# Kernel optimization log

Measured on AMD Instinct MI355X. Metric: run time of the kernel, lower is better.

The kernel has to match this reference:

```python
import jax, jax.numpy as jnp
from jax import lax
import numpy as np

# Hyperparameters (module defaults)
MIP_K = 31
P_LO, P_HI = 0.01, 0.99
ALPHA = 0.15
MU = 10.0
PD_ITERS = 30
TAU = 0.125
SIG_PD = 0.125
THETA = 1.0
EPS = 1e-6


def _forward_grad(u):
    # forward differences, zero-padded on the far edge -> same shape as u
    dx = jnp.pad(u[..., :, 1:] - u[..., :, :-1], ((0, 0), (0, 0), (0, 0), (0, 1)))
    dy = jnp.pad(u[..., 1:, :] - u[..., :-1, :], ((0, 0), (0, 0), (0, 1), (0, 0)))
    return dx, dy


def _divergence(px, py):
    # backward-difference divergence (adjoint of forward grad)
    div_x = px - jnp.pad(px[..., :, :-1], ((0, 0), (0, 0), (0, 0), (1, 0)))
    div_y = py - jnp.pad(py[..., :-1, :], ((0, 0), (0, 0), (1, 0), (0, 0)))
    return div_x + div_y


def _max_pool(x, k):
    # stride-1 max pool with -inf padding (matches torch F.max_pool2d semantics)
    pad = k // 2
    return lax.reduce_window(
        x, -jnp.inf, lax.max,
        window_dimensions=(1, 1, k, k),
        window_strides=(1, 1, 1, 1),
        padding=((0, 0), (0, 0), (pad, pad), (pad, pad)))


def setup_inputs() -> dict:
    key = jax.random.key(0)
    Iy = jax.random.uniform(key, (16, 3, 512, 512), dtype=jnp.float32)
    return {"Iy": Iy}


def reference(Iy):
    R, G, Bc = Iy[:, 0:1], Iy[:, 1:2], Iy[:, 2:3]

    # MIP coarse depth
    Rmax = _max_pool(R, MIP_K)
    GBmax = jnp.maximum(_max_pool(G, MIP_K), _max_pool(Bc, MIP_K))
    x = jnp.abs(Rmax - GBmax) + R

    # robust per-image percentile normalization to [0,1]
    B = x.shape[0]
    flat = x.reshape(B, -1)
    lo = jnp.quantile(flat, P_LO, axis=1)[:, None, None, None]
    hi = jnp.quantile(flat, P_HI, axis=1)[:, None, None, None]
    N_hat = jnp.clip((x - lo) / (hi - lo + EPS), 0.0, 1.0)

    # fixed edge weights from grad(N_hat), sigma = per-image median grad magnitude
    dxh, dyh = _forward_grad(N_hat)
    grad_mag = jnp.sqrt(dxh * dxh + dyh * dyh + EPS)
    sigma = jnp.maximum(
        jnp.quantile(grad_mag.reshape(B, -1), 0.5, axis=1), EPS)[:, None, None, None]
    Wx = 1.0 + MU * jnp.exp(-jnp.abs(dxh) / sigma)
    Wy = 1.0 + MU * jnp.exp(-jnp.abs(dyh) / sigma)

    # Chambolle-Pock primal-dual iterations for weighted TV-L2
    def step(carry, _):
        u, u_bar, px, py = carry
        dx, dy = _forward_grad(u_bar)
        px = jnp.clip(px + SIG_PD * dx, -ALPHA * Wx, ALPHA * Wx)
        py = jnp.clip(py + SIG_PD * dy, -ALPHA * Wy, ALPHA * Wy)
        v = u + TAU * _divergence(px, py)
        u_new = (v + TAU * N_hat) / (1.0 + TAU)
        u_bar = u_new + THETA * (u_new - u)
        return (u_new, u_bar, px, py), None

    z = jnp.zeros_like(N_hat)
    (u, _, _, _), _ = lax.scan(step, (N_hat, N_hat, z, z), None, length=PD_ITERS)
    return jnp.clip(u, 0.0, 1.0)
```

## Files before the change

### kernel.cpp

```cpp
#include <hip/hip_runtime.h>
#include <math.h>

#define B_ 16
#define W_ 512
#define H_ 512
#define S_ (W_*H_)
#define ALPHA_ 0.15f
#define MU_ 10.0f
#define TAU_ 0.125f
#define SIG_ 0.125f
#define EPS_ 1e-6f
#define INV1PT_ (1.0f/(1.0f+TAU_))
#define NBINS 4096
#define BINSCALE 2048.0f
#define BINW (1.0f/2048.0f)

__global__ __launch_bounds__(256) void hmax_kernel(const float* __restrict__ Iy,
                                                   float* __restrict__ Rh,
                                                   float* __restrict__ GBh){
  __shared__ float bufA[2][544], bufB[2][544];
  int t = threadIdx.x;
  int b = blockIdx.x >> 9;
  int i = blockIdx.x & 511;
  const float* row = Iy + (size_t)b*3*S_ + (size_t)i*W_;
  for (int p = t; p < 544; p += 256){
    int idx = p - 16;
    bool v = (idx >= 0) && (idx < 512);
    bufA[0][p] = v ? row[idx] : -1e30f;
    bufA[1][p] = v ? fmaxf(row[S_+idx], row[2*S_+idx]) : -1e30f;
  }
  __syncthreads();
  float (*src)[544] = bufA; float (*dst)[544] = bufB;
  const int ds[5] = {1, 2, 4, 8, 15};
  #pragma unroll
  for (int sstep = 0; sstep < 5; ++sstep){
    int d = ds[sstep];
    for (int p = t; p < 544; p += 256){
      int q = min(p + d, 543);
      dst[0][p] = fmaxf(src[0][p], src[0][q]);
      dst[1][p] = fmaxf(src[1][p], src[1][q]);
    }
    __syncthreads();
    float (*tmp)[544] = src; src = dst; dst = tmp;
  }
  size_t o = (size_t)b*S_ + (size_t)i*W_;
  for (int p = t; p < 512; p += 256){
    Rh[o+p]  = src[0][p+1];
    GBh[o+p] = src[1][p+1];
  }
}

__global__ __launch_bounds__(256) void vscan_fwd_kernel(const float* __restrict__ Rh,
                                                        const float* __restrict__ GBh,
                                                        float* __restrict__ Rf,
                                                        float* __restrict__ Gf){
  int gid = blockIdx.x*256 + threadIdx.x;
  int col = gid & 8191;
  int c   = gid >> 13;
  int b = col >> 9, j = col & 511;
  int i0 = c*31, i1 = min(i0+31, H_);
  size_t base = (size_t)b*S_ + j;
  float rR = -1e30f, rG = -1e30f;
  for (int i = i0; i < i1; ++i){
    size_t o = base + (size_t)i*W_;
    rR = fmaxf(rR, Rh[o]); rG = fmaxf(rG, GBh[o]);
    Rf[o] = rR; Gf[o] = rG;
  }
}

__global__ __launch_bounds__(256) void vscan_bwd_kernel(const float* __restrict__ Rh,
                                                        const float* __restrict__ GBh,
                                                        const float* __restrict__ Rf,
                                                        const float* __restrict__ Gf,
                                                        const float* __restrict__ Iy,
                                                        float* __restrict__ xo,
                                                        unsigned int* __restrict__ hist){
  __shared__ unsigned int h[NBINS];
  int t = threadIdx.x;
  for (int p = t; p < NBINS; p += 256) h[p] = 0u;
  __syncthreads();
  int gid = blockIdx.x*256 + t;
  int col = gid & 8191;
  int c   = gid >> 13;
  int b = col >> 9, j = col & 511;
  int half = j >> 8;
  int i0 = c*31, i1 = min(i0+31, H_);
  size_t base = (size_t)b*S_ + j;
  const float* IyR = Iy + (size_t)b*3*S_ + j;
  float lR = -1e30f, lG = -1e30f;
  for (int i = i1-1; i >= i0; --i){
    size_t o64 = base + (size_t)i*W_;
    lR = fmaxf(lR, Rh[o64]); lG = fmaxf(lG, GBh[o64]);
    int o = i + 15;
    if (o < H_){
      int bi = min(i + 30, H_-1);
      size_t ob = base + (size_t)bi*W_;
      float mR = fmaxf(lR, Rf[ob]);
      float mG = fmaxf(lG, Gf[ob]);
      float xv = fabsf(mR - mG) + IyR[(size_t)o*W_];
      xo[base + (size_t)o*W_] = xv;
      int bin = (int)(xv*BINSCALE);
      bin = min(max(bin, 0), NBINS-1);
      atomicAdd(&h[bin], 1u);
    }
  }
  if (c == 0){
    for (int o = 0; o < 15; ++o){
      size_t ob = base + (size_t)(o+15)*W_;
      float mR = Rf[ob], mG = Gf[ob];
      float xv = fabsf(mR - mG) + IyR[(size_t)o*W_];
      xo[base + (size_t)o*W_] = xv;
      int bin = (int)(xv*BINSCALE);
      bin = min(max(bin, 0), NBINS-1);
      atomicAdd(&h[bin], 1u);
    }
  }
  __syncthreads();
  unsigned int* hb = hist + (size_t)(b*34 + c*2 + half)*NBINS;
  for (int q = t; q < NBINS; q += 256) hb[q] = h[q];
}

__global__ __launch_bounds__(256) void nhat_gmhist_kernel(const float* __restrict__ xb,
                                                          const float* __restrict__ vx2,
                                                          float* __restrict__ nh,
                                                          unsigned int* __restrict__ hist){
  __shared__ unsigned int h[NBINS];
  int t = threadIdx.x;
  int b = blockIdx.x >> 4, sub = blockIdx.x & 15;
  for (int p = t; p < NBINS; p += 256) h[p] = 0u;
  __syncthreads();
  float lo = vx2[2*b], hi = vx2[2*b+1];
  float inv = 1.0f/(hi - lo + EPS_);
  const float* base = xb + (size_t)b*S_;
  float* nhb = nh + (size_t)b*S_;
  int i0 = sub*16384;
  for (int k = 0; k < 64; ++k){
    int idx = i0 + k*256 + t;
    int row = idx >> 9, col = idx & 511;
    float c = fminf(fmaxf((base[idx] - lo)*inv, 0.f), 1.f);
    float dx = 0.f, dy = 0.f;
    if (col < W_-1) dx = fminf(fmaxf((base[idx+1]  - lo)*inv, 0.f), 1.f) - c;
    if (row < H_-1) dy = fminf(fmaxf((base[idx+W_] - lo)*inv, 0.f), 1.f) - c;
    nhb[idx] = c;
    float g = sqrtf(dx*dx + dy*dy + EPS_);
    int bin = (int)(g*BINSCALE);
    bin = min(max(bin, 0), NBINS-1);
    atomicAdd(&h[bin], 1u);
  }
  __syncthreads();
  unsigned int* hb = hist + (size_t)(b*16 + sub)*NBINS;
  for (int q = t; q < NBINS; q += 256) hb[q] = h[q];
}

__global__ __launch_bounds__(256) void pick_hist_kernel(
    const unsigned int* __restrict__ hist, int nsub,
    int r0, int r1, int r2, int r3,
    int nranks, float* __restrict__ outv, int which){
  __shared__ unsigned int part[256];
  __shared__ int s_own[4], s_rem[4];
  __shared__ float s_val[4];
  int t = threadIdx.x, b = blockIdx.x;
  const unsigned int* hb = hist + (size_t)b*nsub*NBINS;
  unsigned int binc[16];
  #pragma unroll
  for (int k = 0; k < 16; ++k) binc[k] = 0u;
  for (int sub = 0; sub < nsub; ++sub){
    const unsigned int* hp = hb + (size_t)sub*NBINS + t*16;
    #pragma unroll
    for (int k = 0; k < 16; ++k) binc[k] += hp[k];
  }
  unsigned int sum = 0u;
  #pragma unroll
  for (int k = 0; k < 16; ++k) sum += binc[k];
  part[t] = sum;
  __syncthreads();
  if (t == 0){
    int rk[4] = {r0, r1, r2, r3};
    for (int ri = 0; ri < nranks; ++ri){
      int rem = rk[ri]; int own = 255;
      for (int q = 0; q < 256; ++q){
        if ((unsigned int)rem < part[q]){ own = q; break; }
        rem -= (int)part[q];
      }
      s_own[ri] = own; s_rem[ri] = rem;
    }
  }
  __syncthreads();
  for (int ri = 0; ri < nranks; ++ri){
    if (t == s_own[ri]){
      int rem = s_rem[ri]; int bin = t*16 + 15;
      #pragma unroll
      for (int q = 0; q < 16; ++q){
        if ((unsigned int)rem < binc[q]){ bin = t*16 + q; break; }
        rem -= (int)binc[q];
      }
      s_val[ri] = ((float)bin + 0.5f) * BINW;
    }
  }
  __syncthreads();
  if (t == 0){
    if (which == 0){
      outv[2*b+0] = s_val[0]*0.57f + s_val[1]*0.43f;
      outv[2*b+1] = s_val[2]*0.43f + s_val[3]*0.57f;
    } else {
      outv[b] = fmaxf(0.5f*(s_val[0] + s_val[1]), EPS_);
    }
  }
}

#define TY 64
#define TX 64
#define HY 10
#define HX 12
#define CY 44
#define CX 40
#define NBY 12
#define NBX 13
#define PSTR 68

#define AW_(d) (ALPHA_*(1.0f + MU_*__expf(-fabsf(d)*invs)))

__global__ __launch_bounds__(1024, 2) void pd_fused_kernel(
    const float* __restrict__ u_in,  const float* __restrict__ ub_in,
    const float* __restrict__ px_in, const float* __restrict__ py_in,
    float* __restrict__ u_out,  float* __restrict__ ub_out,
    float* __restrict__ px_out, float* __restrict__ py_out,
    const float* __restrict__ nh_g, const float* __restrict__ sig_arr,
    int T, int mode)
{
  __shared__ float sA[TY*PSTR], sB[TY*PSTR], sP[TY*PSTR];
  const int t = threadIdx.x;
  const int b = blockIdx.z;
  const int gi0 = blockIdx.y*CY - HY;
  const int gj0 = blockIdx.x*CX - HX;
  const float invs = 1.0f / sig_arr[b];
  const int pi = t >> 4, pj = t & 15;
  const int c0 = 4*pj;
  const int lane = t & 63;
  const size_t bb = (size_t)b*S_;
  const int gi = gi0 + pi;

  #define STAGE(dst, srcP)                                         \
    _Pragma("unroll")                                              \
    for (int k = 0; k < 4; ++k){                                   \
      int p = t + k*1024; int li = p>>6, lj = p & 63;              \
      int sgi = gi0+li, sgj = gj0+lj;                              \
      int gic_ = min(max(sgi,0),H_-1), gjc_ = min(max(sgj,0),W_-1);\
      dst[li*PSTR+lj] = srcP[bb + (size_t)gic_*W_ + gjc_]; }

  if (mode == 1){ STAGE(sA, nh_g) }
  else          { STAGE(sA, ub_in) }

  const int rD = min(pi+1,TY-1);
  const int a_o  = pi*PSTR + c0;
  const int a_up = max(pi-1,0)*PSTR + c0;
  const int a_dn = rD*PSTR + c0;

  int gic  = min(max(gi,0),H_-1);
  int gjc4 = min(max(gj0+c0,0), W_-4);
  size_t go = bb + (size_t)gic*W_ + gjc4;
  float nh_r[4], ax[4], ay[4];
  {
    int giD = min(max(min(gi+1, gi0+TY-1),0),H_-1);
    int gjR = min(max(min(gj0+c0+4, gj0+TX-1),0),W_-1);
    float4 n0 = *(const float4*)&nh_g[go];
    float4 nD = *(const float4*)&nh_g[bb + (size_t)giD*W_ + gjc4];
    float nR = nh_g[bb + (size_t)gic*W_ + gjR];
    float n0a[4] = {n0.x,n0.y,n0.z,n0.w};
    float nDa[4] = {nD.x,nD.y,nD.z,nD.w};
    #pragma unroll
    for (int c = 0; c < 4; ++c){
      nh_r[c] = n0a[c];
      int gj = gj0 + c0 + c;
      float nhR = (c<3) ? n0a[c+1] : nR;
      bool jb = (gj < 0) || (gj >= W_-1);
      ax[c] = jb ? 0.f : AW_(nhR - n0a[c]);
      ay[c] = (gi < 0 || gi >= H_-1) ? 0.f : AW_(nDa[c] - n0a[c]);
    }
  }

  float u_r[4], px_r[4], py_r[4], ub_r[4];
  if (mode == 1){
    #pragma unroll
    for (int c = 0; c < 4; ++c){
      u_r[c] = nh_r[c]; ub_r[c] = nh_r[c];
      px_r[c] = 0.f; py_r[c] = 0.f;
    }
  } else {
    float4 uv  = *(const float4*)&u_in[go];
    float4 pxv = *(const float4*)&px_in[go];
    float4 pyv = *(const float4*)&py_in[go];
    u_r[0]=uv.x;  u_r[1]=uv.y;  u_r[2]=uv.z;  u_r[3]=uv.w;
    px_r[0]=pxv.x; px_r[1]=pxv.y; px_r[2]=pxv.z; px_r[3]=pxv.w;
    py_r[0]=pyv.x; py_r[1]=pyv.y; py_r[2]=pyv.z; py_r[3]=pyv.w;
  }
  __syncthreads();
  if (mode != 1){
    float4 ubv = *(const float4*)&sA[a_o];
    ub_r[0]=ubv.x; ub_r[1]=ubv.y; ub_r[2]=ubv.z; ub_r[3]=ubv.w;
  }

  for (int s = 0; s < T; ++s){
    float* RB = (s & 1) ? sB : sA;
    float* WB = (s & 1) ? sA : sB;
    float4 dn = *(const float4*)&RB[a_dn];
    float ubR = __shfl(ub_r[0], (lane+1)&63);
    if (pj == 15) ubR = ub_r[3];
    float dna[4] = {dn.x,dn.y,dn.z,dn.w};
    #pragma unroll
    for (int c = 0; c < 4; ++c){
      float ubRn = (c<3) ? ub_r[c+1] : ubR;
      px_r[c] = fminf(fmaxf(fmaf(SIG_, ubRn-ub_r[c], px_r[c]), -ax[c]), ax[c]);
      py_r[c] = fminf(fmaxf(fmaf(SIG_, dna[c]-ub_r[c], py_r[c]), -ay[c]), ay[c]);
    }
    *(float4*)&sP[a_o] = make_float4(py_r[0],py_r[1],py_r[2],py_r[3]);
    float pxl3 = __shfl(px_r[3], (lane-1)&63);
    __syncthreads();
    float4 pu = *(const float4*)&sP[a_up];
    float pyu[4] = {pu.x,pu.y,pu.z,pu.w};
    #pragma unroll
    for (int c = 0; c < 4; ++c){
      float pxl = (c>0) ? px_r[c-1] : pxl3;
      float div = px_r[c] + py_r[c] - pxl - pyu[c];
      float un = fmaf(TAU_, div + nh_r[c], u_r[c]) * INV1PT_;
      ub_r[c] = 2.f*un - u_r[c];
      u_r[c] = un;
    }
    if (s < T-1){
      *(float4*)&WB[a_o] = make_float4(ub_r[0],ub_r[1],ub_r[2],ub_r[3]);
      __syncthreads();
    }
  }

  if (pi >= HY && pi < HY+CY && pj >= 3 && pj <= 12 && gi < H_){
    int gj = gj0 + c0;
    if (gj < W_){
      size_t g = bb + (size_t)gi*W_ + gj;
      if (mode == 2){
        *(float4*)&u_out[g] = make_float4(
          fminf(fmaxf(u_r[0],0.f),1.f), fminf(fmaxf(u_r[1],0.f),1.f),
          fminf(fmaxf(u_r[2],0.f),1.f), fminf(fmaxf(u_r[3],0.f),1.f));
      } else {
        *(float4*)&u_out[g]  = make_float4(u_r[0], u_r[1], u_r[2], u_r[3]);
        *(float4*)&ub_out[g] = make_float4(ub_r[0],ub_r[1],ub_r[2],ub_r[3]);
        *(float4*)&px_out[g] = make_float4(px_r[0],px_r[1],px_r[2],px_r[3]);
        *(float4*)&py_out[g] = make_float4(py_r[0],py_r[1],py_r[2],py_r[3]);
      }
    }
  }
}

extern "C" void kernel_launch(void* const* d_in, const int* in_sizes, int n_in,
                              void* d_out, int out_size, void* d_ws, size_t ws_size,
                              hipStream_t stream){
  const float* Iy = (const float*)d_in[0];
  float* out = (float*)d_out;
  char* ws = (char*)d_ws;
  const size_t SLOT = (size_t)B_*S_*sizeof(float);
  float* slot[8];
  for (int q = 0; q < 8; ++q) slot[q] = (float*)(ws + (size_t)q*SLOT);
  float* vx2 = (float*)(ws + (size_t)8*SLOT);
  float* sig = vx2 + 32;

  float* Rh  = slot[0];
  float* GBh = slot[1];
  float* Rf  = slot[5];
  float* Gf  = slot[6];
  float* xb  = slot[2];
  float* nh  = slot[3];
  unsigned int* hist_x  = (unsigned int*)(ws + (size_t)7*SLOT);
  unsigned int* hist_gm = (unsigned int*)(ws + (size_t)7*SLOT + 9437184);

  hmax_kernel<<<B_*H_, 256, 0, stream>>>(Iy, Rh, GBh);
  vscan_fwd_kernel<<<544, 256, 0, stream>>>(Rh, GBh, Rf, Gf);
  vscan_bwd_kernel<<<544, 256, 0, stream>>>(Rh, GBh, Rf, Gf, Iy, xb, hist_x);
  pick_hist_kernel<<<B_, 256, 0, stream>>>(hist_x, 34, 2621, 2622, 259521, 259522, 4, vx2, 0);
  nhat_gmhist_kernel<<<256, 256, 0, stream>>>(xb, vx2, nh, hist_gm);
  pick_hist_kernel<<<B_, 256, 0, stream>>>(hist_gm, 16, 131071, 131072, 0, 0, 2, sig, 1);

  float *uA = slot[1], *ubA = out,     *pxA = slot[5], *pyA = slot[6];
  float *uB = slot[0], *ubB = slot[2], *pxB = slot[7], *pyB = slot[4];

  dim3 pdg(NBX, NBY, B_);
  pd_fused_kernel<<<pdg, 1024, 0, stream>>>(nh, nh, nh, nh,
                                            uA, ubA, pxA, pyA, nh, sig, 10, 1);
  pd_fused_kernel<<<pdg, 1024, 0, stream>>>(uA, ubA, pxA, pyA,
                                            uB, ubB, pxB, pyB, nh, sig, 10, 0);
  pd_fused_kernel<<<pdg, 1024, 0, stream>>>(uB, ubB, pxB, pyB,
                                            out, slot[7], slot[7], slot[7], nh, sig, 10, 2);
}
```

Before: 401.2 us.

## Retile PD temporal blocking to 48x48 cores over four launches, vectorize hmax loads

The primal-dual tile geometry changes from 44x40 output cores with 10/12-pixel halos to 48x48 cores with 8-pixel halos. The 30 iterations are split as 8+8+8+6 across four launches instead of 10+10+10, so the smaller halo still covers the redundant recompute per launch. This cuts the block count and the wasted halo work, but adds one extra round trip of the u/ub/px/py state through global memory. Separately, the hmax row loads become float4, the vertical scan loops get fixed trip counts per chunk, and the workspace slot assignment is reshuffled to fit the extra launch.

New measurement: 380.3 us. 1.06x faster.

```diff
diff --git a/kernel.cpp b/kernel.cpp
--- a/kernel.cpp
+++ b/kernel.cpp
@@ -22,12 +22,22 @@
   int t = threadIdx.x;
   int b = blockIdx.x >> 9;
   int i = blockIdx.x & 511;
-  const float* row = Iy + (size_t)b*3*S_ + (size_t)i*W_;
-  for (int p = t; p < 544; p += 256){
-    int idx = p - 16;
-    bool v = (idx >= 0) && (idx < 512);
-    bufA[0][p] = v ? row[idx] : -1e30f;
-    bufA[1][p] = v ? fmaxf(row[S_+idx], row[2*S_+idx]) : -1e30f;
+  const float* rowR = Iy + (size_t)b*3*S_ + (size_t)i*W_;
+  const float* rowG = rowR + S_;
+  const float* rowB = rowR + 2*S_;
+  if (t < 128){
+    int o4 = (t + 4)*4;
+    float4 r = *(const float4*)&rowR[o4-16];
+    float4 g = *(const float4*)&rowG[o4-16];
+    float4 bb = *(const float4*)&rowB[o4-16];
+    *(float4*)&bufA[0][o4] = r;
+    *(float4*)&bufA[1][o4] = make_float4(fmaxf(g.x,bb.x), fmaxf(g.y,bb.y),
+                                         fmaxf(g.z,bb.z), fmaxf(g.w,bb.w));
+  } else if (t < 160){
+    int e = t - 128;
+    int p = (e < 16) ? e : (512 + e);
+    bufA[0][p] = -1e30f;
+    bufA[1][p] = -1e30f;
   }
   __syncthreads();
   float (*src)[544] = bufA; float (*dst)[544] = bufB;
@@ -58,13 +68,21 @@
   int col = gid & 8191;
   int c   = gid >> 13;
   int b = col >> 9, j = col & 511;
-  int i0 = c*31, i1 = min(i0+31, H_);
+  int i0 = c*31;
   size_t base = (size_t)b*S_ + j;
   float rR = -1e30f, rG = -1e30f;
-  for (int i = i0; i < i1; ++i){
-    size_t o = base + (size_t)i*W_;
-    rR = fmaxf(rR, Rh[o]); rG = fmaxf(rG, GBh[o]);
-    Rf[o] = rR; Gf[o] = rG;
+  if (c <= 15){
+    for (int k = 0; k < 31; ++k){
+      size_t o = base + (size_t)(i0+k)*W_;
+      rR = fmaxf(rR, Rh[o]); rG = fmaxf(rG, GBh[o]);
+      Rf[o] = rR; Gf[o] = rG;
+    }
+  } else {
+    for (int k = 0; k < 16; ++k){
+      size_t o = base + (size_t)(i0+k)*W_;
+      rR = fmaxf(rR, Rh[o]); rG = fmaxf(rG, GBh[o]);
+      Rf[o] = rR; Gf[o] = rG;
+    }
   }
 }
 
@@ -84,24 +102,44 @@
   int c   = gid >> 13;
   int b = col >> 9, j = col & 511;
   int half = j >> 8;
-  int i0 = c*31, i1 = min(i0+31, H_);
+  int i0 = c*31;
   size_t base = (size_t)b*S_ + j;
   const float* IyR = Iy + (size_t)b*3*S_ + j;
   float lR = -1e30f, lG = -1e30f;
-  for (int i = i1-1; i >= i0; --i){
-    size_t o64 = base + (size_t)i*W_;
-    lR = fmaxf(lR, Rh[o64]); lG = fmaxf(lG, GBh[o64]);
-    int o = i + 15;
-    if (o < H_){
-      int bi = min(i + 30, H_-1);
-      size_t ob = base + (size_t)bi*W_;
-      float mR = fmaxf(lR, Rf[ob]);
-      float mG = fmaxf(lG, Gf[ob]);
-      float xv = fabsf(mR - mG) + IyR[(size_t)o*W_];
-      xo[base + (size_t)o*W_] = xv;
-      int bin = (int)(xv*BINSCALE);
-      bin = min(max(bin, 0), NBINS-1);
-      atomicAdd(&h[bin], 1u);
+
+  #define BWD_BODY(I, BI)                                          \
+    { int i_ = (I);                                                \
+      size_t o64 = base + (size_t)i_*W_;                           \
+      lR = fmaxf(lR, Rh[o64]); lG = fmaxf(lG, GBh[o64]);           \
+      int o_ = i_ + 15;                                            \
+      size_t ob = base + (size_t)(BI)*W_;                          \
+      float mR = fmaxf(lR, Rf[ob]);                                \
+      float mG = fmaxf(lG, Gf[ob]);                                \
+      float xv = fabsf(mR - mG) + IyR[(size_t)o_*W_];              \
+      xo[base + (size_t)o_*W_] = xv;                               \
+      int bin = (int)(xv*BINSCALE);                                \
+      bin = min(max(bin, 0), NBINS-1);                             \
+      atomicAdd(&h[bin], 1u); }
+
+  if (c <= 14){
+    for (int k = 30; k >= 0; --k) BWD_BODY(i0+k, i0+k+30)
+  } else if (c == 15){
+    for (int k = 30; k >= 0; --k) BWD_BODY(i0+k, min(i0+k+30, H_-1))
+  } else {
+    for (int i = H_-1; i >= i0; --i){
+      size_t o64 = base + (size_t)i*W_;
+      lR = fmaxf(lR, Rh[o64]); lG = fmaxf(lG, GBh[o64]);
+      int o = i + 15;
+      if (o < H_){
+        size_t ob = base + (size_t)(H_-1)*W_;
+        float mR = fmaxf(lR, Rf[ob]);
+        float mG = fmaxf(lG, Gf[ob]);
+        float xv = fabsf(mR - mG) + IyR[(size_t)o*W_];
+        xo[base + (size_t)o*W_] = xv;
+        int bin = (int)(xv*BINSCALE);
+        bin = min(max(bin, 0), NBINS-1);
+        atomicAdd(&h[bin], 1u);
+      }
     }
   }
   if (c == 0){
@@ -210,12 +248,12 @@
 
 #define TY 64
 #define TX 64
-#define HY 10
-#define HX 12
-#define CY 44
-#define CX 40
-#define NBY 12
-#define NBX 13
+#define HY 8
+#define HX 8
+#define CY 48
+#define CX 48
+#define NBY 11
+#define NBX 11
 #define PSTR 68
 
 #define AW_(d) (ALPHA_*(1.0f + MU_*__expf(-fabsf(d)*invs)))
@@ -332,7 +370,7 @@
     }
   }
 
-  if (pi >= HY && pi < HY+CY && pj >= 3 && pj <= 12 && gi < H_){
+  if (pi >= HY && pi < HY+CY && pj >= HX/4 && pj < (HX+CX)/4 && gi < H_){
     int gj = gj0 + c0;
     if (gj < W_){
       size_t g = bb + (size_t)gi*W_ + gj;
@@ -368,8 +406,8 @@
   float* Gf  = slot[6];
   float* xb  = slot[2];
   float* nh  = slot[3];
-  unsigned int* hist_x  = (unsigned int*)(ws + (size_t)7*SLOT);
-  unsigned int* hist_gm = (unsigned int*)(ws + (size_t)7*SLOT + 9437184);
+  unsigned int* hist_x  = (unsigned int*)(ws + (size_t)4*SLOT);
+  unsigned int* hist_gm = (unsigned int*)(ws + (size_t)4*SLOT + 9437184);
 
   hmax_kernel<<<B_*H_, 256, 0, stream>>>(Iy, Rh, GBh);
   vscan_fwd_kernel<<<544, 256, 0, stream>>>(Rh, GBh, Rf, Gf);
@@ -378,14 +416,16 @@
   nhat_gmhist_kernel<<<256, 256, 0, stream>>>(xb, vx2, nh, hist_gm);
   pick_hist_kernel<<<B_, 256, 0, stream>>>(hist_gm, 16, 131071, 131072, 0, 0, 2, sig, 1);
 
-  float *uA = slot[1], *ubA = out,     *pxA = slot[5], *pyA = slot[6];
-  float *uB = slot[0], *ubB = slot[2], *pxB = slot[7], *pyB = slot[4];
+  float *uA = slot[1], *ubA = slot[2], *pxA = slot[5], *pyA = slot[6];
+  float *uB = slot[0], *ubB = slot[4], *pxB = slot[7], *pyB = out;
 
   dim3 pdg(NBX, NBY, B_);
   pd_fused_kernel<<<pdg, 1024, 0, stream>>>(nh, nh, nh, nh,
-                                            uA, ubA, pxA, pyA, nh, sig, 10, 1);
+                                            uA, ubA, pxA, pyA, nh, sig, 8, 1);
   pd_fused_kernel<<<pdg, 1024, 0, stream>>>(uA, ubA, pxA, pyA,
-                                            uB, ubB, pxB, pyB, nh, sig, 10, 0);
+                                            uB, ubB, pxB, pyB, nh, sig, 8, 0);
   pd_fused_kernel<<<pdg, 1024, 0, stream>>>(uB, ubB, pxB, pyB,
-                                            out, slot[7], slot[7], slot[7], nh, sig, 10, 2);
-}
+                                            uA, ubA, pxA, pyA, nh, sig, 8, 0);
+  pd_fused_kernel<<<pdg, 1024, 0, stream>>>(uA, ubA, pxA, pyA,
+                                            out, slot[7], slot[7], slot[7], nh, sig, 6, 2);
+}
```
